# Optimization experiments

Hardware: AMD Instinct MI355X
Metric: run time of the kernel (lower is better)

Reference implementation:

```python
import jax, jax.numpy as jnp
import numpy as np

N_ATOMS = 51200
N_MOL = 512
FEAT = 384


def setup_inputs() -> dict:
    key = jax.random.key(0)
    ks = jax.random.split(key, 20)
    s = 0.05  # small random weights instead of the degenerate zero-init
    inp = {
        "node_feats": jax.random.normal(ks[0], (N_ATOMS, FEAT), jnp.float32),
        "energy": jax.random.normal(ks[1], (N_MOL,), jnp.float32),
        "forces": jax.random.normal(ks[2], (N_ATOMS, 3), jnp.float32),
        "stress": jax.random.normal(ks[3], (N_MOL, 3, 3), jnp.float32),
        "W1": jax.random.normal(ks[4], (64, 256), jnp.float32) * s,
        "b1": jnp.zeros((64,), jnp.float32),
        "W2": jax.random.normal(ks[5], (16, 64), jnp.float32) * s,
        "b2": jnp.zeros((16,), jnp.float32),
        "W3": jax.random.normal(ks[6], (1, 16), jnp.float32) * s,
        "b3": jnp.zeros((1,), jnp.float32),
        "W1f": jax.random.normal(ks[7], (64, 256), jnp.float32) * s,
        "b1f": jnp.zeros((64,), jnp.float32),
        "W2f": jax.random.normal(ks[8], (16, 64), jnp.float32) * s,
        "b2f": jnp.zeros((16,), jnp.float32),
        "W3f": jax.random.normal(ks[9], (1, 16), jnp.float32) * s,
        "b3f": jnp.zeros((1,), jnp.float32),
        "S_uncert": jnp.zeros((1,), jnp.float32),
        # atom -> molecule segment ids (sorted, every molecule non-empty)
        "batch_idx": jnp.repeat(jnp.arange(N_MOL, dtype=jnp.int64), N_ATOMS // N_MOL),
    }
    return inp


def _mlp(x, W1, b1, W2, b2, W3, b3):
    h = jax.nn.silu(x @ W1.T + b1)
    h = jax.nn.silu(h @ W2.T + b2)
    return h @ W3.T + b3  # [N, 1]


def reference(node_feats, energy, forces, stress,
              W1, b1, W2, b2, W3, b3,
              W1f, b1f, W2f, b2f, W3f, b3f,
              S_uncert, batch_idx):
    # concat first 128 and last 128 feature channels -> [N, 256]
    nf = jnp.concatenate([node_feats[:, :128], node_feats[:, -128:]], axis=1)

    # E head: faithfully zeroed out and replaced by constant 0.6
    e_stds = jnp.exp(_mlp(nf, W1, b1, W2, b2, W3, b3))[:, 0] * 0 + 0.6  # [N]
    # F head
    f_u = jnp.exp(_mlp(nf, W1f, b1f, W2f, b2f, W3f, b3f))[:, 0] * 0.1   # [N]
    force_uncert = jnp.stack([f_u, f_u, f_u], axis=-1)                  # [N, 3]
    # stress uncert: constant 0.1/16 (S_uncert term zeroed, kept faithfully)
    stress_uncert = jnp.ones_like(stress) * jnp.exp(S_uncert[0]) * 0 + 0.1 / 16

    # per-molecule mean of e_stds via segment sums (scatter_add in torch)
    eu_sum = jax.ops.segment_sum(e_stds, batch_idx, num_segments=N_MOL)
    n_atoms = jax.ops.segment_sum(jnp.ones_like(e_stds), batch_idx, num_segments=N_MOL)
    energy_uncert = eu_sum / n_atoms  # [n_mol]

    return (energy, forces, stress, energy_uncert, force_uncert, stress_uncert)
```

## Files before the change

kernel.cpp:

```cpp
#include <hip/hip_runtime.h>
#include <hip/hip_bf16.h>

#define N_ATOMS 51200
#define FEAT    384

#define OUT_FUNC   159232
#define COPY_TOTAL 163840

typedef __attribute__((ext_vector_type(4))) float f32x4;
typedef __attribute__((ext_vector_type(4))) short s16x4;
typedef __attribute__((ext_vector_type(8))) short s16x8;

constexpr int BLK = 256;

__device__ __forceinline__ short f2bf(float x) {
    union { __hip_bfloat16 b; short s; } u;
    u.b = __float2bfloat16(x);
    return u.s;
}
__device__ __forceinline__ float silu_(float v) {
    return v / (1.0f + __expf(-v));
}

__global__ __launch_bounds__(BLK) void funcert_kernel(
    const float* __restrict__ nf,
    const float* __restrict__ energy,
    const float* __restrict__ forces,
    const float* __restrict__ stress,
    const float* __restrict__ W1f, const float* __restrict__ b1f,
    const float* __restrict__ W2f, const float* __restrict__ b2f,
    const float* __restrict__ W3f, const float* __restrict__ b3f,
    float* __restrict__ out)
{
    const int t   = threadIdx.x;
    const int gid = blockIdx.x * BLK + t;

    if (gid < COPY_TOTAL) {
        float v; int o = gid;
        if      (gid < 512)    { v = energy[gid]; }
        else if (gid < 154112) { v = forces[gid - 512]; }
        else if (gid < 158720) { v = stress[gid - 154112]; }
        else if (gid < 159232) { v = 0.6f; }
        else                   { v = 0.1f / 16.0f; o = gid + 153600; }
        out[o] = v;
    }

    __shared__ short Xs[64 * 256];
    __shared__ short H1s[64 * 64];

    const int lane  = t & 63;
    const int w     = t >> 6;
    const int g     = lane >> 4;
    const int col   = lane & 15;
    const int abase = blockIdx.x * 64;

    const int ch = w * 16 + col;
    s16x8 wfrag[8];
    #pragma unroll
    for (int ks = 0; ks < 8; ++ks) {
        const float* p = W1f + ch * 256 + ks * 32 + g * 8;
        const f32x4 lo = *(const f32x4*)p;
        const f32x4 hi = *(const f32x4*)(p + 4);
        s16x8 f;
        f[0]=f2bf(lo.x); f[1]=f2bf(lo.y); f[2]=f2bf(lo.z); f[3]=f2bf(lo.w);
        f[4]=f2bf(hi.x); f[5]=f2bf(hi.y); f[6]=f2bf(hi.z); f[7]=f2bf(hi.w);
        wfrag[ks] = f;
    }
    const float b1v = b1f[ch];

    #pragma unroll
    for (int i = 0; i < 16; ++i) {
        const int r  = i * 4 + w;
        const int g4 = lane + (lane >= 32 ? 32 : 0);
        const f32x4 x = ((const f32x4*)nf)[(size_t)(abase + r) * 96 + g4];
        const int sp = (lane >> 1) ^ (r & 7);
        s16x4 b; b.x=f2bf(x.x); b.y=f2bf(x.y); b.z=f2bf(x.z); b.w=f2bf(x.w);
        *(s16x4*)(Xs + r * 256 + sp * 8 + (lane & 1) * 4) = b;
    }
    __syncthreads();

    #pragma unroll
    for (int mt = 0; mt < 4; ++mt) {
        const int row = mt * 16 + col;
        f32x4 a = {0.f, 0.f, 0.f, 0.f};
        #pragma unroll
        for (int ks = 0; ks < 8; ++ks) {
            const int sp = (ks * 4 + g) ^ (row & 7);
            const s16x8 af = *(const s16x8*)(Xs + row * 256 + sp * 8);
            a = __builtin_amdgcn_mfma_f32_16x16x32_bf16(af, wfrag[ks], a, 0, 0, 0);
        }
        #pragma unroll
        for (int r = 0; r < 4; ++r) {
            const int atom = mt * 16 + g * 4 + r;
            H1s[atom * 64 + ch] = f2bf(silu_(a[r] + b1v));
        }
    }
    __syncthreads();

    s16x8 w2frag[2];
    #pragma unroll
    for (int ks = 0; ks < 2; ++ks) {
        const float* p = W2f + col * 64 + ks * 32 + g * 8;
        const f32x4 lo = *(const f32x4*)p;
        const f32x4 hi = *(const f32x4*)(p + 4);
        s16x8 f;
        f[0]=f2bf(lo.x); f[1]=f2bf(lo.y); f[2]=f2bf(lo.z); f[3]=f2bf(lo.w);
        f[4]=f2bf(hi.x); f[5]=f2bf(hi.y); f[6]=f2bf(hi.z); f[7]=f2bf(hi.w);
        w2frag[ks] = f;
    }
    const int arow = w * 16 + col;
    f32x4 a2 = {0.f, 0.f, 0.f, 0.f};
    #pragma unroll
    for (int ks = 0; ks < 2; ++ks) {
        const s16x8 af = *(const s16x8*)(H1s + arow * 64 + ks * 32 + g * 8);
        a2 = __builtin_amdgcn_mfma_f32_16x16x32_bf16(af, w2frag[ks], a2, 0, 0, 0);
    }

    const float b2v = b2f[col];
    const float w3v = W3f[col];
    float y[4];
    #pragma unroll
    for (int r = 0; r < 4; ++r)
        y[r] = silu_(a2[r] + b2v) * w3v;
    #pragma unroll
    for (int m = 1; m < 16; m <<= 1) {
        #pragma unroll
        for (int r = 0; r < 4; ++r)
            y[r] += __shfl_xor(y[r], m, 64);
    }
    const float b3v = b3f[0];
    float fu[4];
    #pragma unroll
    for (int r = 0; r < 4; ++r)
        fu[r] = __expf(y[r] + b3v) * 0.1f;

    if (col < 12) {
        const int a_ = col / 3, c = col - a_ * 3;
        const float v = (a_ == 0) ? fu[0] : (a_ == 1) ? fu[1] : (a_ == 2) ? fu[2] : fu[3];
        const int atom = w * 16 + g * 4 + a_;
        out[OUT_FUNC + 3 * (abase + atom) + c] = v;
    }
}

extern "C" void kernel_launch(void* const* d_in, const int* in_sizes, int n_in,
                              void* d_out, int out_size, void* d_ws, size_t ws_size,
                              hipStream_t stream) {
    const float* nf     = (const float*)d_in[0];
    const float* energy = (const float*)d_in[1];
    const float* forces = (const float*)d_in[2];
    const float* stress = (const float*)d_in[3];
    const float* W1f    = (const float*)d_in[10];
    const float* b1f    = (const float*)d_in[11];
    const float* W2f    = (const float*)d_in[12];
    const float* b2f    = (const float*)d_in[13];
    const float* W3f    = (const float*)d_in[14];
    const float* b3f    = (const float*)d_in[15];
    float* out = (float*)d_out;

    dim3 grid(N_ATOMS / 64);
    funcert_kernel<<<grid, BLK, 0, stream>>>(nf, energy, forces, stress,
                                             W1f, b1f, W2f, b2f, W3f, b3f, out);
}
```

Measured before the change: 23.92 us.

## Give each wave its own 16 atoms and load activations directly into MFMA fragments

Each wave now owns 16 atoms and loads its node-feature rows straight from global memory into bf16 A-fragments held in registers. This removes the 32KB shared X staging buffer and both block-wide barriers. W1 is streamed from global (L2-resident) per output tile instead of being held as per-wave register fragments. The H1 intermediate goes to a per-wave XOR-swizzled LDS slice, and launch bounds request 4 blocks per CU. This trades less LDS traffic and synchronisation, and higher occupancy, for repeated W1 reads and conversions in every wave plus less coalesced row-strided activation loads.

After: 43.72 us. 1.83x slower.

```diff
diff --git a/kernel.cpp b/kernel.cpp
--- a/kernel.cpp
+++ b/kernel.cpp
@@ -2,13 +2,11 @@
 #include <hip/hip_bf16.h>
 
 #define N_ATOMS 51200
-#define FEAT    384
 
 #define OUT_FUNC   159232
 #define COPY_TOTAL 163840
 
 typedef __attribute__((ext_vector_type(4))) float f32x4;
-typedef __attribute__((ext_vector_type(4))) short s16x4;
 typedef __attribute__((ext_vector_type(8))) short s16x8;
 
 constexpr int BLK = 256;
@@ -18,11 +16,15 @@
     u.b = __float2bfloat16(x);
     return u.s;
 }
-__device__ __forceinline__ float silu_(float v) {
-    return v / (1.0f + __expf(-v));
+__device__ __forceinline__ float silu_(float v) { return v / (1.0f + __expf(-v)); }
+__device__ __forceinline__ s16x8 cvt8(f32x4 lo, f32x4 hi) {
+    s16x8 f;
+    f[0]=f2bf(lo.x); f[1]=f2bf(lo.y); f[2]=f2bf(lo.z); f[3]=f2bf(lo.w);
+    f[4]=f2bf(hi.x); f[5]=f2bf(hi.y); f[6]=f2bf(hi.z); f[7]=f2bf(hi.w);
+    return f;
 }
 
-__global__ __launch_bounds__(BLK) void funcert_kernel(
+__global__ __launch_bounds__(BLK, 4) void funcert_kernel(
     const float* __restrict__ nf,
     const float* __restrict__ energy,
     const float* __restrict__ forces,
@@ -45,75 +47,66 @@
         out[o] = v;
     }
 
-    __shared__ short Xs[64 * 256];
-    __shared__ short H1s[64 * 64];
+    __shared__ short H1s[4 * 1024];
 
-    const int lane  = t & 63;
-    const int w     = t >> 6;
-    const int g     = lane >> 4;
-    const int col   = lane & 15;
-    const int abase = blockIdx.x * 64;
+    const int lane = t & 63;
+    const int w    = t >> 6;
+    const int g    = lane >> 4;
+    const int col  = lane & 15;
+    const int awave = blockIdx.x * 64 + w * 16;
 
-    const int ch = w * 16 + col;
-    s16x8 wfrag[8];
+    f32x4 xv[16];
     #pragma unroll
     for (int ks = 0; ks < 8; ++ks) {
-        const float* p = W1f + ch * 256 + ks * 32 + g * 8;
-        const f32x4 lo = *(const f32x4*)p;
-        const f32x4 hi = *(const f32x4*)(p + 4);
-        s16x8 f;
-        f[0]=f2bf(lo.x); f[1]=f2bf(lo.y); f[2]=f2bf(lo.z); f[3]=f2bf(lo.w);
-        f[4]=f2bf(hi.x); f[5]=f2bf(hi.y); f[6]=f2bf(hi.z); f[7]=f2bf(hi.w);
-        wfrag[ks] = f;
+        const int kb = ks * 32 + g * 8;
+        const int fb = kb + (kb >= 128 ? 128 : 0);
+        const float* p = nf + (size_t)(awave + col) * 384 + fb;
+        xv[2 * ks]     = *(const f32x4*)p;
+        xv[2 * ks + 1] = *(const f32x4*)(p + 4);
     }
-    const float b1v = b1f[ch];
+    s16x8 afrag[8];
+    #pragma unroll
+    for (int ks = 0; ks < 8; ++ks)
+        afrag[ks] = cvt8(xv[2 * ks], xv[2 * ks + 1]);
+
+    short* Hw = H1s + w * 1024;
 
     #pragma unroll
-    for (int i = 0; i < 16; ++i) {
-        const int r  = i * 4 + w;
-        const int g4 = lane + (lane >= 32 ? 32 : 0);
-        const f32x4 x = ((const f32x4*)nf)[(size_t)(abase + r) * 96 + g4];
-        const int sp = (lane >> 1) ^ (r & 7);
-        s16x4 b; b.x=f2bf(x.x); b.y=f2bf(x.y); b.z=f2bf(x.z); b.w=f2bf(x.w);
-        *(s16x4*)(Xs + r * 256 + sp * 8 + (lane & 1) * 4) = b;
-    }
-    __syncthreads();
-
-    #pragma unroll
-    for (int mt = 0; mt < 4; ++mt) {
-        const int row = mt * 16 + col;
-        f32x4 a = {0.f, 0.f, 0.f, 0.f};
+    for (int nt = 0; nt < 4; ++nt) {
+        const int ch = nt * 16 + col;
+        f32x4 acc = {0.f, 0.f, 0.f, 0.f};
         #pragma unroll
-        for (int ks = 0; ks < 8; ++ks) {
-            const int sp = (ks * 4 + g) ^ (row & 7);
-            const s16x8 af = *(const s16x8*)(Xs + row * 256 + sp * 8);
-            a = __builtin_amdgcn_mfma_f32_16x16x32_bf16(af, wfrag[ks], a, 0, 0, 0);
+        for (int h = 0; h < 2; ++h) {
+            f32x4 bv[8];
+            #pragma unroll
+            for (int k4 = 0; k4 < 4; ++k4) {
+                const int ks = h * 4 + k4;
+                const float* p = W1f + ch * 256 + ks * 32 + g * 8;
+                bv[2 * k4]     = *(const f32x4*)p;
+                bv[2 * k4 + 1] = *(const f32x4*)(p + 4);
+            }
+            #pragma unroll
+            for (int k4 = 0; k4 < 4; ++k4)
+                acc = __builtin_amdgcn_mfma_f32_16x16x32_bf16(
+                        afrag[h * 4 + k4], cvt8(bv[2 * k4], bv[2 * k4 + 1]), acc, 0, 0, 0);
         }
+        const float b1v = b1f[ch];
         #pragma unroll
         for (int r = 0; r < 4; ++r) {
-            const int atom = mt * 16 + g * 4 + r;
-            H1s[atom * 64 + ch] = f2bf(silu_(a[r] + b1v));
+            const int a = g * 4 + r;
+            *(short*)((char*)Hw + a * 128 + ((ch * 2) ^ ((a & 7) << 4))) =
+                f2bf(silu_(acc[r] + b1v));
         }
     }
-    __syncthreads();
 
-    s16x8 w2frag[2];
+    f32x4 acc2 = {0.f, 0.f, 0.f, 0.f};
     #pragma unroll
-    for (int ks = 0; ks < 2; ++ks) {
-        const float* p = W2f + col * 64 + ks * 32 + g * 8;
-        const f32x4 lo = *(const f32x4*)p;
-        const f32x4 hi = *(const f32x4*)(p + 4);
-        s16x8 f;
-        f[0]=f2bf(lo.x); f[1]=f2bf(lo.y); f[2]=f2bf(lo.z); f[3]=f2bf(lo.w);
-        f[4]=f2bf(hi.x); f[5]=f2bf(hi.y); f[6]=f2bf(hi.z); f[7]=f2bf(hi.w);
-        w2frag[ks] = f;
-    }
-    const int arow = w * 16 + col;
-    f32x4 a2 = {0.f, 0.f, 0.f, 0.f};
-    #pragma unroll
-    for (int ks = 0; ks < 2; ++ks) {
-        const s16x8 af = *(const s16x8*)(H1s + arow * 64 + ks * 32 + g * 8);
-        a2 = __builtin_amdgcn_mfma_f32_16x16x32_bf16(af, w2frag[ks], a2, 0, 0, 0);
+    for (int ks2 = 0; ks2 < 2; ++ks2) {
+        const float* p = W2f + col * 64 + ks2 * 32 + g * 8;
+        const s16x8 bf2 = cvt8(*(const f32x4*)p, *(const f32x4*)(p + 4));
+        const s16x8 af2 = *(const s16x8*)((char*)Hw + col * 128 +
+                                          ((ks2 * 64 + g * 16) ^ ((col & 7) << 4)));
+        acc2 = __builtin_amdgcn_mfma_f32_16x16x32_bf16(af2, bf2, acc2, 0, 0, 0);
     }
 
     const float b2v = b2f[col];
@@ -121,7 +114,7 @@
     float y[4];
     #pragma unroll
     for (int r = 0; r < 4; ++r)
-        y[r] = silu_(a2[r] + b2v) * w3v;
+        y[r] = silu_(acc2[r] + b2v) * w3v;
     #pragma unroll
     for (int m = 1; m < 16; m <<= 1) {
         #pragma unroll
@@ -137,8 +130,7 @@
     if (col < 12) {
         const int a_ = col / 3, c = col - a_ * 3;
         const float v = (a_ == 0) ? fu[0] : (a_ == 1) ? fu[1] : (a_ == 2) ? fu[2] : fu[3];
-        const int atom = w * 16 + g * 4 + a_;
-        out[OUT_FUNC + 3 * (abase + atom) + c] = v;
+        out[OUT_FUNC + 3 * (awave + g * 4 + a_) + c] = v;
     }
 }
 
```
